# Optimization experiments

Measured on AMD Instinct MI355X. Metric: run time of the kernel, lower is better.

The kernel has to match this reference:

```python
import jax, jax.numpy as jnp
import numpy as np

BATCH, SEQ, IN, HID, OUT = 128, 1024, 256, 512, 256


def setup_inputs() -> dict:
    key = jax.random.key(0)
    k_x, k_wi, k_bi, k_wo, k_bo = jax.random.split(key, 5)
    # torch.nn.Linear default init: U(-1/sqrt(fan_in), 1/sqrt(fan_in))
    s_i = 1.0 / np.sqrt(IN + HID)
    s_o = 1.0 / np.sqrt(HID)
    return {
        "x": jax.random.normal(k_x, (BATCH, SEQ, IN), dtype=jnp.float32),
        "W_i2h": jax.random.uniform(k_wi, (HID, IN + HID), jnp.float32, -s_i, s_i),
        "b_i2h": jax.random.uniform(k_bi, (HID,), jnp.float32, -s_i, s_i),
        "W_h2o": jax.random.uniform(k_wo, (OUT, HID), jnp.float32, -s_o, s_o),
        "b_h2o": jax.random.uniform(k_bo, (OUT,), jnp.float32, -s_o, s_o),
    }


def reference(x, W_i2h, b_i2h, W_h2o, b_h2o):
    batch = x.shape[0]
    hid = W_i2h.shape[0]
    # Split i2h weight into input and hidden blocks: cat(x_t, h) @ W.T == x_t @ Wx.T + h @ Wh.T
    Wx = W_i2h[:, : x.shape[-1]]  # (hid, in)
    Wh = W_i2h[:, x.shape[-1] :]  # (hid, hid)
    # Precompute input contributions for all timesteps in one GEMM: (B,S,hid)
    xW = jnp.einsum("bsi,hi->bsh", x, Wx) + b_i2h

    def step(h, xw_t):
        h_new = jnp.tanh(xw_t + h @ Wh.T)
        return h_new, h_new

    h0 = jnp.zeros((batch, hid), dtype=x.dtype)
    h_last, hs = jax.lax.scan(step, h0, jnp.swapaxes(xW, 0, 1))  # hs: (S,B,hid)
    hs = jnp.swapaxes(hs, 0, 1)  # (B,S,hid)
    outputs = jnp.einsum("bsh,oh->bso", hs, W_h2o) + b_h2o  # (B,S,out)
    return outputs, h_last
```

## Files before the change

kernel.cpp:

```cpp
#include <hip/hip_runtime.h>

typedef __attribute__((ext_vector_type(8))) short bf16frag;
typedef __attribute__((ext_vector_type(4))) float f32x4;

constexpr int B = 128, S = 1024, DI = 256, DH = 512, DO = 256;
constexpr int MAXNB = 16;
constexpr size_t OUT_MAIN = (size_t)B * S * DO;
constexpr size_t SLOT_BYTES = (size_t)B * DH * 2;
constexpr size_t FLAGS_BYTES = 8 * 2 * MAXNB * 64;
constexpr int WH_OFF = 0;
constexpr int WX_OFF = 16384;
constexpr int WHO_OFF = 24576;
constexpr int LDS_BYTES = 65536;

__device__ __forceinline__ void release_vm() {
  asm volatile("s_waitcnt vmcnt(0)" ::: "memory");
}
__device__ __forceinline__ void acquire_cc() {
  asm volatile("" ::: "memory");
}

__device__ __forceinline__ unsigned short f2bf(float f) {
  unsigned int u = __float_as_uint(f);
  u += 0x7fffu + ((u >> 16) & 1u);
  return (unsigned short)(u >> 16);
}
__device__ __forceinline__ float bf2f(unsigned short h) {
  return __uint_as_float(((unsigned int)h) << 16);
}
__device__ __forceinline__ float fast_tanh(float x) {
  float e = __expf(2.0f * x);
  return 1.0f - 2.0f * __builtin_amdgcn_rcpf(e + 1.0f);
}
__device__ __forceinline__ bf16frag cvt8(float4 a, float4 b) {
  bf16frag r;
  r[0]=(short)f2bf(a.x); r[1]=(short)f2bf(a.y); r[2]=(short)f2bf(a.z); r[3]=(short)f2bf(a.w);
  r[4]=(short)f2bf(b.x); r[5]=(short)f2bf(b.y); r[6]=(short)f2bf(b.z); r[7]=(short)f2bf(b.w);
  return r;
}
__device__ __forceinline__ bf16frag load8(const void* base, size_t off, bool fp32m) {
  if (fp32m) {
    const float4* p = reinterpret_cast<const float4*>((const float*)base + off);
    return cvt8(p[0], p[1]);
  }
  return *reinterpret_cast<const bf16frag*>((const unsigned short*)base + off);
}

__device__ __forceinline__ void wait2(const int* a1, int t1, const int* a2, int t2) {
  int guard = 0;
  while (true) {
    int v1 = __hip_atomic_load(a1, __ATOMIC_RELAXED, __HIP_MEMORY_SCOPE_AGENT);
    int v2 = __hip_atomic_load(a2, __ATOMIC_RELAXED, __HIP_MEMORY_SCOPE_AGENT);
    if (v1 >= t1 && v2 >= t2) break;
    if (++guard > (1 << 26)) break;
    __builtin_amdgcn_s_sleep(1);
  }
}

__global__ void __launch_bounds__(192, 1)
rnn_persistent(const void* __restrict__ xv,
               const void* __restrict__ Wi2hv,
               const void* __restrict__ biv,
               const void* __restrict__ Whov,
               const void* __restrict__ bov,
               void* __restrict__ outv,
               unsigned short* __restrict__ hbuf,
               int* __restrict__ flags,
               int nm, int lg) {
  extern __shared__ unsigned short lds[];
  const int tid = threadIdx.x;
  const int lane = tid & 63;
  const int wave = tid >> 6;
  const int blk = blockIdx.x;
  const int c   = blk & 7;
  const int mem = blk >> 3;
  const int b0  = c * 16;
  const int n_base = mem * 32;
  const int o_base = mem * 16;

  bool fp32m;
  {
    const unsigned short* xu = (const unsigned short*)xv;
    int c0 = 0;
    for (int i = lane; i < 4096; i += 64)
      c0 += (((xu[i] >> 7) & 0xFF) >= 0xC0);
    #pragma unroll
    for (int s = 32; s; s >>= 1) c0 += __shfl_xor(c0, s, 64);
    fp32m = (c0 > 100);
  }

  for (int i = tid; i < 32 * 64; i += 192) {
    int r = i >> 6, bk = i & 63;
    bf16frag v = load8(Wi2hv, (size_t)(n_base + r) * 768 + 256 + bk * 8, fp32m);
    *reinterpret_cast<bf16frag*>(lds + WH_OFF + r * 512 + ((bk ^ (r & 7)) * 8)) = v;
  }
  for (int i = tid; i < 32 * 32; i += 192) {
    int r = i >> 5, bk = i & 31;
    bf16frag v = load8(Wi2hv, (size_t)(n_base + r) * 768 + bk * 8, fp32m);
    *reinterpret_cast<bf16frag*>(lds + WX_OFF + r * 256 + ((bk ^ (r & 7)) * 8)) = v;
  }
  for (int i = tid; i < 16 * 64; i += 192) {
    int r = i >> 6, bk = i & 63;
    bf16frag v = load8(Whov, (size_t)(o_base + r) * 512 + bk * 8, fp32m);
    *reinterpret_cast<bf16frag*>(lds + WHO_OFF + r * 512 + ((bk ^ (r & 7)) * 8)) = v;
  }
  __syncthreads();

  int* cnt = flags + c * (2 * MAXNB * 16);
  const int q  = lane >> 4;
  const int ln = lane & 15;
  float* outf = (float*)outv;
  unsigned short* outh = (unsigned short*)outv;

  if (wave < 2) {
    const int nlB  = wave * 16 + ln;
    const int n_g  = n_base + nlB;
    const float bias = fp32m ? ((const float*)biv)[n_g]
                             : bf2f(((const unsigned short*)biv)[n_g]);
    const int swz = nlB & 7;
    const size_t xrow = (size_t)(b0 + ln) * (S * DI) + q * 8;
    const size_t hrow_off = (size_t)(b0 + ln) * DH + q * 8;

    bf16frag xf[8];
    #pragma unroll
    for (int cc = 0; cc < 8; ++cc)
      xf[cc] = load8(xv, xrow + cc * 32, fp32m);

    for (int t = 0; t < S; ++t) {
      f32x4 acc = {bias, bias, bias, bias};
      #pragma unroll
      for (int cc = 0; cc < 8; ++cc) {
        bf16frag wf = *reinterpret_cast<const bf16frag*>(
            lds + WX_OFF + nlB * 256 + (((cc * 4 + q) ^ swz) * 8));
        acc = __builtin_amdgcn_mfma_f32_16x16x32_bf16(xf[cc], wf, acc, 0, 0, 0);
      }
      if (t + 1 < S) {
        #pragma unroll
        for (int cc = 0; cc < 8; ++cc)
          xf[cc] = load8(xv, xrow + (size_t)(t + 1) * DI + cc * 32, fp32m);
      }
      if (t > 0) {
        const int* a1 = cnt + ((t - 1) & nm) * 16;
        int th1 = 32 * (((t - 1) >> lg) + 1);
        const int* a2 = a1;
        int th2 = th1;
        if (t > nm) { a2 = cnt + (MAXNB + (t & nm)) * 16; th2 = 16 * (t >> lg); }
        wait2(a1, th1, a2, th2);
        acquire_cc();
        const unsigned short* hsrc = hbuf + (size_t)((t - 1) & nm) * (B * DH) + hrow_off;
        unsigned long long hlo[16], hhi[16];
        #pragma unroll
        for (int cc = 0; cc < 16; ++cc) {
          const unsigned long long* p = reinterpret_cast<const unsigned long long*>(hsrc + cc * 32);
          hlo[cc] = __hip_atomic_load(p,     __ATOMIC_RELAXED, __HIP_MEMORY_SCOPE_AGENT);
          hhi[cc] = __hip_atomic_load(p + 1, __ATOMIC_RELAXED, __HIP_MEMORY_SCOPE_AGENT);
        }
        #pragma unroll
        for (int cc = 0; cc < 16; ++cc) {
          union { unsigned long long u[2]; bf16frag f; } cvt;
          cvt.u[0] = hlo[cc]; cvt.u[1] = hhi[cc];
          bf16frag wf = *reinterpret_cast<const bf16frag*>(
              lds + WH_OFF + nlB * 512 + (((cc * 4 + q) ^ swz) * 8));
          acc = __builtin_amdgcn_mfma_f32_16x16x32_bf16(cvt.f, wf, acc, 0, 0, 0);
        }
      }
      unsigned short* hdst = hbuf + (size_t)(t & nm) * (B * DH);
      #pragma unroll
      for (int r = 0; r < 4; ++r) {
        float hv = fast_tanh(acc[r]);
        unsigned short hu = f2bf(hv);
        unsigned int other = __shfl_xor((unsigned int)hu, 1, 64);
        if ((lane & 1) == 0) {
          unsigned int packed = (unsigned int)hu | (other << 16);
          __hip_atomic_store(reinterpret_cast<unsigned int*>(
              hdst + (size_t)(b0 + q * 4 + r) * DH + n_g),
              packed, __ATOMIC_RELAXED, __HIP_MEMORY_SCOPE_AGENT);
        }
        if (t == S - 1) {
          size_t hidx = OUT_MAIN + (size_t)(b0 + q * 4 + r) * DH + n_g;
          if (fp32m) outf[hidx] = hv; else outh[hidx] = hu;
        }
      }
      release_vm();
      if (lane == 0)
        __hip_atomic_fetch_add(cnt + (t & nm) * 16, 1,
                               __ATOMIC_RELAXED, __HIP_MEMORY_SCOPE_AGENT);
    }
  } else {
    const int o_g = o_base + ln;
    const float bias = fp32m ? ((const float*)bov)[o_g]
                             : bf2f(((const unsigned short*)bov)[o_g]);
    const int swz = ln & 7;
    const size_t hrow_off = (size_t)(b0 + ln) * DH + q * 8;
    for (int u = 0; u < S; ++u) {
      const int* a1 = cnt + (u & nm) * 16;
      int th1 = 32 * ((u >> lg) + 1);
      wait2(a1, th1, a1, th1);
      acquire_cc();
      const unsigned short* hsrc = hbuf + (size_t)(u & nm) * (B * DH) + hrow_off;
      unsigned long long hlo[16], hhi[16];
      #pragma unroll
      for (int cc = 0; cc < 16; ++cc) {
        const unsigned long long* p = reinterpret_cast<const unsigned long long*>(hsrc + cc * 32);
        hlo[cc] = __hip_atomic_load(p,     __ATOMIC_RELAXED, __HIP_MEMORY_SCOPE_AGENT);
        hhi[cc] = __hip_atomic_load(p + 1, __ATOMIC_RELAXED, __HIP_MEMORY_SCOPE_AGENT);
      }
      f32x4 acc = {bias, bias, bias, bias};
      #pragma unroll
      for (int cc = 0; cc < 16; ++cc) {
        union { unsigned long long u[2]; bf16frag f; } cvt;
        cvt.u[0] = hlo[cc]; cvt.u[1] = hhi[cc];
        bf16frag wf = *reinterpret_cast<const bf16frag*>(
            lds + WHO_OFF + ln * 512 + (((cc * 4 + q) ^ swz) * 8));
        acc = __builtin_amdgcn_mfma_f32_16x16x32_bf16(cvt.f, wf, acc, 0, 0, 0);
      }
      #pragma unroll
      for (int r = 0; r < 4; ++r) {
        size_t oidx = ((size_t)(b0 + q * 4 + r) * S + u) * DO + o_g;
        if (fp32m) outf[oidx] = acc[r]; else outh[oidx] = f2bf(acc[r]);
      }
      release_vm();
      if (lane == 0)
        __hip_atomic_fetch_add(cnt + (MAXNB + (u & nm)) * 16, 1,
                               __ATOMIC_RELAXED, __HIP_MEMORY_SCOPE_AGENT);
    }
  }
}

extern "C" void kernel_launch(void* const* d_in, const int* in_sizes, int n_in,
                              void* d_out, int out_size, void* d_ws, size_t ws_size,
                              hipStream_t stream) {
  const void* x    = d_in[0];
  const void* Wi2h = d_in[1];
  const void* bi   = d_in[2];
  const void* Who  = d_in[3];
  const void* bo   = d_in[4];
  void* out = d_out;

  int nb = MAXNB;
  while ((size_t)nb * SLOT_BYTES + FLAGS_BYTES > ws_size && nb > 4) nb >>= 1;
  if ((size_t)nb * SLOT_BYTES + FLAGS_BYTES > ws_size) return;
  int nm = nb - 1;
  int lg = (nb == 16) ? 4 : (nb == 8) ? 3 : 2;

  unsigned short* hbuf = (unsigned short*)d_ws;
  int* flags = (int*)((char*)d_ws + (size_t)nb * SLOT_BYTES);

  hipMemsetAsync(flags, 0, FLAGS_BYTES, stream);

  void* args[] = { (void*)&x, (void*)&Wi2h, (void*)&bi, (void*)&Who, (void*)&bo,
                   (void*)&out, (void*)&hbuf, (void*)&flags, (void*)&nm, (void*)&lg };
  hipError_t e = hipLaunchCooperativeKernel((void*)rnn_persistent, dim3(128), dim3(192),
                                            args, LDS_BYTES, stream);
  if (e != hipSuccess) {
    rnn_persistent<<<dim3(128), dim3(192), LDS_BYTES, stream>>>(
        x, Wi2h, bi, Who, bo, out, hbuf, flags, nm, lg);
  }
}
```

Before: 8.835 ms.

## Use cache-bypassing dwordx4 h loads, split MFMA chains, release slot earlier

Replaces the paired 64-bit atomic loads of the hidden state with inline-asm global_load_dwordx4 using sc0 sc1 cache bypass, so each fragment takes one wide load. Splits the 16-long MFMA accumulation into two interleaved accumulator chains to shorten the dependent-MFMA latency. The output waves now signal slot consumption right after loading h, before computing and storing outputs, which loosens the ring-buffer backpressure on the recurrence waves. The early signal drops the vmcnt wait on output stores. It relies on the asm cache bits to give coherent reads, and the changed summation order can shift rounding slightly.

```diff
diff --git a/kernel.cpp b/kernel.cpp
--- a/kernel.cpp
+++ b/kernel.cpp
@@ -2,6 +2,7 @@
 
 typedef __attribute__((ext_vector_type(8))) short bf16frag;
 typedef __attribute__((ext_vector_type(4))) float f32x4;
+typedef __attribute__((ext_vector_type(4))) unsigned int u32x4;
 
 constexpr int B = 128, S = 1024, DI = 256, DH = 512, DO = 256;
 constexpr int MAXNB = 16;
@@ -55,6 +56,17 @@
     if (++guard > (1 << 26)) break;
     __builtin_amdgcn_s_sleep(1);
   }
+}
+
+__device__ __forceinline__ void hload16(const unsigned short* hsrc, u32x4* hv) {
+  #pragma unroll
+  for (int cc = 0; cc < 16; ++cc) {
+    const unsigned short* p = hsrc + cc * 32;
+    asm volatile("global_load_dwordx4 %0, %1, off sc0 sc1"
+                 : "=v"(hv[cc]) : "v"(p) : "memory");
+  }
+  asm volatile("s_waitcnt vmcnt(0)" ::: "memory");
+  __builtin_amdgcn_sched_barrier(0);
 }
 
 __global__ void __launch_bounds__(192, 1)
@@ -148,27 +160,24 @@
         wait2(a1, th1, a2, th2);
         acquire_cc();
         const unsigned short* hsrc = hbuf + (size_t)((t - 1) & nm) * (B * DH) + hrow_off;
-        unsigned long long hlo[16], hhi[16];
+        u32x4 hv[16];
+        hload16(hsrc, hv);
+        f32x4 acc2 = {0.f, 0.f, 0.f, 0.f};
         #pragma unroll
         for (int cc = 0; cc < 16; ++cc) {
-          const unsigned long long* p = reinterpret_cast<const unsigned long long*>(hsrc + cc * 32);
-          hlo[cc] = __hip_atomic_load(p,     __ATOMIC_RELAXED, __HIP_MEMORY_SCOPE_AGENT);
-          hhi[cc] = __hip_atomic_load(p + 1, __ATOMIC_RELAXED, __HIP_MEMORY_SCOPE_AGENT);
-        }
-        #pragma unroll
-        for (int cc = 0; cc < 16; ++cc) {
-          union { unsigned long long u[2]; bf16frag f; } cvt;
-          cvt.u[0] = hlo[cc]; cvt.u[1] = hhi[cc];
+          union { u32x4 u; bf16frag f; } cv; cv.u = hv[cc];
           bf16frag wf = *reinterpret_cast<const bf16frag*>(
               lds + WH_OFF + nlB * 512 + (((cc * 4 + q) ^ swz) * 8));
-          acc = __builtin_amdgcn_mfma_f32_16x16x32_bf16(cvt.f, wf, acc, 0, 0, 0);
+          if (cc & 1) acc2 = __builtin_amdgcn_mfma_f32_16x16x32_bf16(cv.f, wf, acc2, 0, 0, 0);
+          else        acc  = __builtin_amdgcn_mfma_f32_16x16x32_bf16(cv.f, wf, acc,  0, 0, 0);
         }
+        acc += acc2;
       }
       unsigned short* hdst = hbuf + (size_t)(t & nm) * (B * DH);
       #pragma unroll
       for (int r = 0; r < 4; ++r) {
-        float hv = fast_tanh(acc[r]);
-        unsigned short hu = f2bf(hv);
+        float hvf = fast_tanh(acc[r]);
+        unsigned short hu = f2bf(hvf);
         unsigned int other = __shfl_xor((unsigned int)hu, 1, 64);
         if ((lane & 1) == 0) {
           unsigned int packed = (unsigned int)hu | (other << 16);
@@ -178,7 +187,7 @@
         }
         if (t == S - 1) {
           size_t hidx = OUT_MAIN + (size_t)(b0 + q * 4 + r) * DH + n_g;
-          if (fp32m) outf[hidx] = hv; else outh[hidx] = hu;
+          if (fp32m) outf[hidx] = hvf; else outh[hidx] = hu;
         }
       }
       release_vm();
@@ -198,31 +207,27 @@
       wait2(a1, th1, a1, th1);
       acquire_cc();
       const unsigned short* hsrc = hbuf + (size_t)(u & nm) * (B * DH) + hrow_off;
-      unsigned long long hlo[16], hhi[16];
+      u32x4 hv[16];
+      hload16(hsrc, hv);
+      if (lane == 0)
+        __hip_atomic_fetch_add(cnt + (MAXNB + (u & nm)) * 16, 1,
+                               __ATOMIC_RELAXED, __HIP_MEMORY_SCOPE_AGENT);
+      f32x4 acc = {bias, bias, bias, bias};
+      f32x4 acc2 = {0.f, 0.f, 0.f, 0.f};
       #pragma unroll
       for (int cc = 0; cc < 16; ++cc) {
-        const unsigned long long* p = reinterpret_cast<const unsigned long long*>(hsrc + cc * 32);
-        hlo[cc] = __hip_atomic_load(p,     __ATOMIC_RELAXED, __HIP_MEMORY_SCOPE_AGENT);
-        hhi[cc] = __hip_atomic_load(p + 1, __ATOMIC_RELAXED, __HIP_MEMORY_SCOPE_AGENT);
-      }
-      f32x4 acc = {bias, bias, bias, bias};
-      #pragma unroll
-      for (int cc = 0; cc < 16; ++cc) {
-        union { unsigned long long u[2]; bf16frag f; } cvt;
-        cvt.u[0] = hlo[cc]; cvt.u[1] = hhi[cc];
+        union { u32x4 u; bf16frag f; } cv; cv.u = hv[cc];
         bf16frag wf = *reinterpret_cast<const bf16frag*>(
             lds + WHO_OFF + ln * 512 + (((cc * 4 + q) ^ swz) * 8));
-        acc = __builtin_amdgcn_mfma_f32_16x16x32_bf16(cvt.f, wf, acc, 0, 0, 0);
-      }
+        if (cc & 1) acc2 = __builtin_amdgcn_mfma_f32_16x16x32_bf16(cv.f, wf, acc2, 0, 0, 0);
+        else        acc  = __builtin_amdgcn_mfma_f32_16x16x32_bf16(cv.f, wf, acc,  0, 0, 0);
+      }
+      acc += acc2;
       #pragma unroll
       for (int r = 0; r < 4; ++r) {
         size_t oidx = ((size_t)(b0 + q * 4 + r) * S + u) * DO + o_g;
         if (fp32m) outf[oidx] = acc[r]; else outh[oidx] = f2bf(acc[r]);
       }
-      release_vm();
-      if (lane == 0)
-        __hip_atomic_fetch_add(cnt + (MAXNB + (u & nm)) * 16, 1,
-                               __ATOMIC_RELAXED, __HIP_MEMORY_SCOPE_AGENT);
     }
   }
 }
```

Result: faster. 7.804 ms (-11.7%).
